# Performance work log

Measured on AMD Instinct MI355X. Metric: run time of the kernel, lower is better.

## Reference

```python
import jax, jax.numpy as jnp
import numpy as np

E = 80000   # number of directed edges
T = 80000   # number of triplets
HID = 256   # hidden_channels
INT = 64    # int_emb_size == num_bilinear
NR = 6      # num_radial
NS = 7      # num_spherical
BD = 8      # basis_emb_size_dist
BA = 8      # basis_emb_size_angle


def swish(x):
    return x * jax.nn.sigmoid(x)


def setup_inputs() -> dict:
    key = jax.random.key(0)
    ks = jax.random.split(key, 16)
    inp = {
        "x1": jax.random.normal(ks[0], (E, HID), dtype=jnp.float32),
        "rbf0": jax.random.normal(ks[1], (E, NR), dtype=jnp.float32),
        "sbf": jax.random.normal(ks[2], (T, NS * NR), dtype=jnp.float32),
        "t": jax.random.normal(ks[3], (T, NS * NS * NR), dtype=jnp.float32),
        "x_kj": jax.random.normal(ks[4], (E, HID), dtype=jnp.float32),
        "x_ji": jax.random.normal(ks[5], (E, HID), dtype=jnp.float32),
        "idx_kj": jax.random.randint(ks[6], (T,), 0, E, dtype=jnp.int32),
        "idx_ji": jax.random.randint(ks[7], (T,), 0, E, dtype=jnp.int32),
        # weights stored [in, out] so y = x @ W (torch Linear uses weight.T)
        "W_rbf1": jax.random.normal(ks[8], (NR, BD), dtype=jnp.float32) * 0.3,
        "W_rbf2": jax.random.normal(ks[9], (BD, HID), dtype=jnp.float32) * 0.3,
        "W_sbf1": jax.random.normal(ks[10], (NS * NR, BA), dtype=jnp.float32) * 0.15,
        "W_sbf2": jax.random.normal(ks[11], (BA, INT), dtype=jnp.float32) * 0.3,
        "W_t1": jax.random.normal(ks[12], (NS * NS * NR, INT), dtype=jnp.float32) * 0.06,
        "W_down": jax.random.normal(ks[13], (HID, INT), dtype=jnp.float32) * 0.06,
        "W_up": jax.random.normal(ks[14], (INT, HID), dtype=jnp.float32) * 0.12,
        # bilinear weight W: [int_emb, num_bilinear, int_emb], std = 2/int_emb
        "W_bil": jax.random.normal(ks[15], (INT, INT, INT), dtype=jnp.float32) * (2.0 / INT),
    }
    return inp


def reference(x1, rbf0, sbf, t, x_kj, x_ji, idx_kj, idx_ji,
              W_rbf1, W_rbf2, W_sbf1, W_sbf2, W_t1, W_down, W_up, W_bil):
    # rbf projection: [E, NR] -> [E, HID]
    rbf = (rbf0 @ W_rbf1) @ W_rbf2
    xk = x_kj * rbf                          # [E, HID]
    xk = swish(xk @ W_down)                  # [E, INT]
    # sbf projection: [T, NS*NR] -> [T, INT]
    s = (sbf @ W_sbf1) @ W_sbf2
    xk = xk[idx_kj] * s                      # gather to triplets: [T, INT]
    tt = t @ W_t1                            # [T, INT] (num_bilinear dim)
    # bilinear: 'wj,wl,ijl->wi' with W_bil [INT(i), INT(j), INT(l)]
    a = jnp.einsum('wj,ijl->wil', tt, W_bil)  # [T, INT, INT]
    out_t = jnp.einsum('wil,wl->wi', a, xk)   # [T, INT]
    # scatter-add triplets back to edges
    agg = jax.ops.segment_sum(out_t, idx_ji, num_segments=x1.shape[0])  # [E, INT]
    return swish(agg @ W_up)                  # [E, HID]
```

## Files before the change

### kernel.cpp

```cpp
#include <hip/hip_runtime.h>
#include <hip/hip_fp16.h>

#define E_N 80000
#define T_N 80000

typedef _Float16 h4 __attribute__((ext_vector_type(4)));
typedef _Float16 h8 __attribute__((ext_vector_type(8)));
typedef float    f4 __attribute__((ext_vector_type(4)));
typedef float    f2 __attribute__((ext_vector_type(2)));
typedef unsigned int u4 __attribute__((ext_vector_type(4)));

static __device__ __forceinline__ float swishf(float x) {
    return x / (1.0f + __expf(-x));
}

__global__ __launch_bounds__(256) void kp_pack(const float* __restrict__ Wb,
                                               h8* __restrict__ wpack) {
    int g = blockIdx.x * 256 + threadIdx.x;
    int i    = ((g >> 6) & 3) * 16 + (g & 15);
    int c    = (g >> 8) & 1;
    int j    = g >> 9;
    int quad = (g >> 4) & 3;
    int l0   = c * 32 + quad * 8;
    const float* src = Wb + ((i * 64 + j) << 6) + l0;
    h8 v;
#pragma unroll
    for (int u = 0; u < 8; ++u) v[u] = (_Float16)src[u];
    wpack[g] = v;
}

__global__ __launch_bounds__(256) void kpack_w(const float* __restrict__ src,
                                               h8* __restrict__ dst,
                                               int Ksrc, int N, int NT) {
    int g = blockIdx.x * 256 + threadIdx.x;
    int lane = g & 63, frag = g >> 6;
    int nt = frag % NT, kt = frag / NT;
    int quad = (lane >> 4);
    int n = nt * 16 + (lane & 15);
    int k0 = kt * 32 + quad * 8;
    h8 v;
#pragma unroll
    for (int u = 0; u < 8; ++u) {
        int k = k0 + u;
        v[u] = (k < Ksrc) ? (_Float16)src[(size_t)k * N + n] : (_Float16)0.0f;
    }
    dst[g] = v;
}

__global__ __launch_bounds__(256) void k1_down(const float* __restrict__ rbf0,
                                               const float* __restrict__ xkj,
                                               const float* __restrict__ W_rbf1,
                                               const float* __restrict__ W_rbf2,
                                               const h8* __restrict__ wpd,
                                               _Float16* __restrict__ xke) {
    int tid = threadIdx.x;
    int lane = tid & 63, wv = tid >> 6;
    int m = lane & 15, quad = lane >> 4;
    int rowb = blockIdx.x * 128 + wv * 32;

    float r8[2][8];
#pragma unroll
    for (int rt = 0; rt < 2; ++rt) {
        int r = rowb + rt * 16 + m;
        float rv[6];
#pragma unroll
        for (int q = 0; q < 6; ++q) rv[q] = rbf0[(size_t)r * 6 + q];
#pragma unroll
        for (int p = 0; p < 8; ++p) {
            float s = 0.f;
#pragma unroll
            for (int q = 0; q < 6; ++q) s += rv[q] * W_rbf1[q * 8 + p];
            r8[rt][p] = s;
        }
    }

    f4 acc[2][4] = {};
    for (int kb = 0; kb < 4; ++kb) {
#pragma unroll
        for (int kt = 0; kt < 2; ++kt) {
            int k0 = kb * 64 + kt * 32 + quad * 8;
            f4 w2lo[8], w2hi[8];
#pragma unroll
            for (int p = 0; p < 8; ++p) {
                w2lo[p] = *(const f4*)(W_rbf2 + p * 256 + k0);
                w2hi[p] = *(const f4*)(W_rbf2 + p * 256 + k0 + 4);
            }
            h8 afrag[2];
#pragma unroll
            for (int rt = 0; rt < 2; ++rt) {
                size_t base = (size_t)(rowb + rt * 16 + m) * 256 + k0;
                f4 xlo = *(const f4*)(xkj + base);
                f4 xhi = *(const f4*)(xkj + base + 4);
                f4 rlo = {}, rhi = {};
#pragma unroll
                for (int p = 0; p < 8; ++p) {
                    rlo += r8[rt][p] * w2lo[p];
                    rhi += r8[rt][p] * w2hi[p];
                }
                rlo *= xlo; rhi *= xhi;
                h8 a;
#pragma unroll
                for (int u = 0; u < 4; ++u) {
                    a[u]     = (_Float16)rlo[u];
                    a[u + 4] = (_Float16)rhi[u];
                }
                afrag[rt] = a;
            }
#pragma unroll
            for (int nt = 0; nt < 4; ++nt) {
                h8 b = wpd[(((kb * 2 + kt) * 4 + nt) << 6) + lane];
#pragma unroll
                for (int rt = 0; rt < 2; ++rt)
                    acc[rt][nt] = __builtin_amdgcn_mfma_f32_16x16x32_f16(afrag[rt], b, acc[rt][nt], 0, 0, 0);
            }
        }
    }

#pragma unroll
    for (int rt = 0; rt < 2; ++rt)
#pragma unroll
        for (int nt = 0; nt < 4; ++nt)
#pragma unroll
            for (int rr = 0; rr < 4; ++rr) {
                int row = rowb + rt * 16 + quad * 4 + rr;
                xke[(size_t)row * 64 + nt * 16 + m] = (_Float16)swishf(acc[rt][nt][rr]);
            }
}

__global__ __launch_bounds__(256) void kb1_tproj(const float* __restrict__ tin,
                                                 const h8* __restrict__ wpt,
                                                 _Float16* __restrict__ ttb) {
    int tid = threadIdx.x;
    int lane = tid & 63, wv = tid >> 6;
    int m = lane & 15, quad = lane >> 4;
    int rowb = blockIdx.x * 128 + wv * 32;

    f4 acc[2][4] = {};
    for (int ktg = 0; ktg < 10; ++ktg) {
        int k0 = ktg * 32 + quad * 8;
        h8 afrag[2];
#pragma unroll
        for (int rt = 0; rt < 2; ++rt) {
            size_t base = (size_t)(rowb + rt * 16 + m) * 294 + k0;
            h8 a;
            if (k0 + 8 <= 294) {
                f2 t0 = *(const f2*)(tin + base);
                f2 t1 = *(const f2*)(tin + base + 2);
                f2 t2 = *(const f2*)(tin + base + 4);
                f2 t3 = *(const f2*)(tin + base + 6);
                a[0] = (_Float16)t0[0]; a[1] = (_Float16)t0[1];
                a[2] = (_Float16)t1[0]; a[3] = (_Float16)t1[1];
                a[4] = (_Float16)t2[0]; a[5] = (_Float16)t2[1];
                a[6] = (_Float16)t3[0]; a[7] = (_Float16)t3[1];
            } else {
#pragma unroll
                for (int u = 0; u < 8; ++u) {
                    int k = k0 + u;
                    a[u] = (k < 294) ? (_Float16)tin[base + u] : (_Float16)0.0f;
                }
            }
            afrag[rt] = a;
        }
#pragma unroll
        for (int nt = 0; nt < 4; ++nt) {
            h8 b = wpt[((ktg * 4 + nt) << 6) + lane];
#pragma unroll
            for (int rt = 0; rt < 2; ++rt)
                acc[rt][nt] = __builtin_amdgcn_mfma_f32_16x16x32_f16(afrag[rt], b, acc[rt][nt], 0, 0, 0);
        }
    }

#pragma unroll
    for (int rt = 0; rt < 2; ++rt)
#pragma unroll
        for (int nt = 0; nt < 4; ++nt)
#pragma unroll
            for (int rr = 0; rr < 4; ++rr) {
                int row = rowb + rt * 16 + quad * 4 + rr;
                ttb[(size_t)row * 64 + nt * 16 + m] = (_Float16)acc[rt][nt][rr];
            }
}

__global__ __launch_bounds__(256) void kb2_gather(const float* __restrict__ sbf,
                                                  const float* __restrict__ W_sbf1,
                                                  const float* __restrict__ W_sbf2,
                                                  const _Float16* __restrict__ xke,
                                                  const int* __restrict__ idx_kj,
                                                  _Float16* __restrict__ xkt) {
    __shared__ float sbfL[32 * 42];
    __shared__ float midL[32 * 8];
    int tid = threadIdx.x;
    int row0 = blockIdx.x * 32;
    for (int i = tid; i < 32 * 42; i += 256)
        sbfL[i] = sbf[(size_t)row0 * 42 + i];
    __syncthreads();
    {
        int r = tid >> 3, p = tid & 7;
        float mm = 0.f;
#pragma unroll
        for (int q = 0; q < 42; ++q) mm += sbfL[r * 42 + q] * W_sbf1[q * 8 + p];
        midL[r * 8 + p] = mm;
    }
    __syncthreads();
    int r = tid >> 3;
    int c0 = (tid & 7) * 8;
    int w = row0 + r;
    int e = idx_kj[w];
    f4 sa = {}, sb = {};
#pragma unroll
    for (int p = 0; p < 8; ++p) {
        float mm = midL[r * 8 + p];
        sa += mm * *(const f4*)(W_sbf2 + (p << 6) + c0);
        sb += mm * *(const f4*)(W_sbf2 + (p << 6) + c0 + 4);
    }
    h8 xv = *(const h8*)(xke + (size_t)e * 64 + c0);
    h8 o;
#pragma unroll
    for (int u = 0; u < 4; ++u) {
        o[u]     = (_Float16)((float)xv[u]     * sa[u]);
        o[u + 4] = (_Float16)((float)xv[u + 4] * sb[u]);
    }
    *(h8*)(xkt + (size_t)w * 64 + c0) = o;
}

__global__ __launch_bounds__(256, 2) void kb3_bilinear(const _Float16* __restrict__ xkt,
                                                       const _Float16* __restrict__ ttp,
                                                       const h8* __restrict__ wpack,
                                                       const int* __restrict__ idx_ji,
                                                       float* __restrict__ agg) {
    __shared__ _Float16 xktL[256 * 72];
    __shared__ _Float16 ttL[256 * 72];
    int tid = threadIdx.x;
    int lane = tid & 63, wv = tid >> 6;
    int qrow = lane & 15, quad = lane >> 4;
    int row0 = blockIdx.x * 256;
    int jlo = blockIdx.y * 32;

#pragma unroll
    for (int pass = 0; pass < 8; ++pass) {
        int r = pass * 32 + (tid >> 3);
        int part = tid & 7;
        int gr = row0 + r;
        u4 vx = {0, 0, 0, 0}, vt = {0, 0, 0, 0};
        if (gr < T_N) {
            vx = *(const u4*)(xkt + (size_t)gr * 64 + part * 8);
            vt = *(const u4*)(ttp + (size_t)gr * 64 + part * 8);
        }
        *(u4*)&xktL[r * 72 + part * 8] = vx;
        *(u4*)&ttL[r * 72 + part * 8] = vt;
    }
    __syncthreads();

    int wrow = wv * 64;
    h8 xa[4][2];
#pragma unroll
    for (int rt = 0; rt < 4; ++rt)
#pragma unroll
        for (int c = 0; c < 2; ++c)
            xa[rt][c] = *(const h8*)&xktL[(wrow + rt * 16 + qrow) * 72 + c * 32 + quad * 8];

    f4 acc[4][4] = {};
    for (int j = jlo; j < jlo + 32; ++j) {
        h8 bf[2][4];
#pragma unroll
        for (int c = 0; c < 2; ++c)
#pragma unroll
            for (int nt = 0; nt < 4; ++nt)
                bf[c][nt] = wpack[(((j * 2 + c) * 4 + nt) << 6) + lane];
        _Float16 tv[4];
#pragma unroll
        for (int rt = 0; rt < 4; ++rt)
            tv[rt] = ttL[(wrow + rt * 16 + qrow) * 72 + j];
#pragma unroll
        for (int rt = 0; rt < 4; ++rt) {
            h8 t8 = {tv[rt], tv[rt], tv[rt], tv[rt], tv[rt], tv[rt], tv[rt], tv[rt]};
            h8 a0 = xa[rt][0] * t8;
            h8 a1 = xa[rt][1] * t8;
#pragma unroll
            for (int nt = 0; nt < 4; ++nt) {
                acc[rt][nt] = __builtin_amdgcn_mfma_f32_16x16x32_f16(a0, bf[0][nt], acc[rt][nt], 0, 0, 0);
                acc[rt][nt] = __builtin_amdgcn_mfma_f32_16x16x32_f16(a1, bf[1][nt], acc[rt][nt], 0, 0, 0);
            }
        }
    }

#pragma unroll
    for (int rt = 0; rt < 4; ++rt) {
#pragma unroll
        for (int rr = 0; rr < 4; ++rr) {
            int w = row0 + wrow + rt * 16 + quad * 4 + rr;
            if (w < T_N) {
                int e = idx_ji[w];
                float* dst = agg + (size_t)e * 64 + qrow;
#pragma unroll
                for (int nt = 0; nt < 4; ++nt)
                    atomicAdd(dst + nt * 16, acc[rt][nt][rr]);
            }
        }
    }
}

__global__ __launch_bounds__(256) void k4_up(const float* __restrict__ agg,
                                             const h8* __restrict__ wpu,
                                             float* __restrict__ out) {
    int tid = threadIdx.x;
    int lane = tid & 63, wv = tid >> 6;
    int m = lane & 15, quad = lane >> 4;
    int rowb = blockIdx.x * 64 + wv * 16;

    f4 acc[16] = {};
#pragma unroll
    for (int kt = 0; kt < 2; ++kt) {
        const float* ap = agg + (size_t)(rowb + m) * 64 + kt * 32 + quad * 8;
        f4 alo = *(const f4*)ap;
        f4 ahi = *(const f4*)(ap + 4);
        h8 a;
#pragma unroll
        for (int u = 0; u < 4; ++u) {
            a[u]     = (_Float16)alo[u];
            a[u + 4] = (_Float16)ahi[u];
        }
#pragma unroll
        for (int nt = 0; nt < 16; ++nt) {
            h8 b = wpu[((kt * 16 + nt) << 6) + lane];
            acc[nt] = __builtin_amdgcn_mfma_f32_16x16x32_f16(a, b, acc[nt], 0, 0, 0);
        }
    }

#pragma unroll
    for (int nt = 0; nt < 16; ++nt)
#pragma unroll
        for (int rr = 0; rr < 4; ++rr) {
            int row = rowb + quad * 4 + rr;
            out[(size_t)row * 256 + nt * 16 + m] = swishf(acc[nt][rr]);
        }
}

extern "C" void kernel_launch(void* const* d_in, const int* in_sizes, int n_in,
                              void* d_out, int out_size, void* d_ws, size_t ws_size,
                              hipStream_t stream) {
    const float* rbf0   = (const float*)d_in[1];
    const float* sbf    = (const float*)d_in[2];
    const float* tin    = (const float*)d_in[3];
    const float* xkj    = (const float*)d_in[4];
    const int*   idx_kj = (const int*)d_in[6];
    const int*   idx_ji = (const int*)d_in[7];
    const float* W_rbf1 = (const float*)d_in[8];
    const float* W_rbf2 = (const float*)d_in[9];
    const float* W_sbf1 = (const float*)d_in[10];
    const float* W_sbf2 = (const float*)d_in[11];
    const float* W_t1   = (const float*)d_in[12];
    const float* W_down = (const float*)d_in[13];
    const float* W_up   = (const float*)d_in[14];
    const float* W_bil  = (const float*)d_in[15];

    char* ws = (char*)d_ws;
    _Float16* xke = (_Float16*)ws;
    float*    agg = (float*)(ws + 10240000);
    h8* wpack_bil = (h8*)(ws + 30720000);
    h8* wpd       = (h8*)(ws + 31244288);
    h8* wpt       = (h8*)(ws + 31277056);
    h8* wpu       = (h8*)(ws + 31318016);
    _Float16* ttb = (_Float16*)d_out;
    _Float16* xkt = (_Float16*)((char*)d_out + 10240000);
    float*    out = (float*)d_out;

    kp_pack<<<128, 256, 0, stream>>>(W_bil, wpack_bil);
    kpack_w<<<8,  256, 0, stream>>>(W_down, wpd, 256, 64, 4);
    kpack_w<<<10, 256, 0, stream>>>(W_t1,   wpt, 294, 64, 4);
    kpack_w<<<8,  256, 0, stream>>>(W_up,   wpu, 64, 256, 16);
    k1_down<<<625, 256, 0, stream>>>(rbf0, xkj, W_rbf1, W_rbf2, wpd, xke);
    kb1_tproj<<<625, 256, 0, stream>>>(tin, wpt, ttb);
    kb2_gather<<<2500, 256, 0, stream>>>(sbf, W_sbf1, W_sbf2, xke, idx_kj, xkt);
    hipMemsetAsync(agg, 0, (size_t)E_N * 64 * 4, stream);
    kb3_bilinear<<<dim3(313, 2), 256, 0, stream>>>(xkt, ttb, wpack_bil, idx_ji, agg);
    k4_up<<<1250, 256, 0, stream>>>(agg, wpu, out);
}
```

Baseline: 479.8 us.

## Merge weight-pack kernels, drop LDS staging in bilinear, flatten down-proj loop

Packs all four weight tensors in one kernel launch instead of four, which cuts launch overhead. The bilinear kernel now uses 128-thread blocks that read xkt and tt fragments straight from global memory instead of staging them in shared memory, and it loads eight tt values at a time per row. The bounds check on T goes away because 625*128 rows covers T exactly. k1_down unrolls its K loop fully under a launch bound of 4, and the memset moves earlier in the stream. The risks are higher register pressure and uncoalesced global reads in the bilinear kernel.

```diff
diff --git a/kernel.cpp b/kernel.cpp
--- a/kernel.cpp
+++ b/kernel.cpp
@@ -14,25 +14,9 @@
     return x / (1.0f + __expf(-x));
 }
 
-__global__ __launch_bounds__(256) void kp_pack(const float* __restrict__ Wb,
-                                               h8* __restrict__ wpack) {
-    int g = blockIdx.x * 256 + threadIdx.x;
-    int i    = ((g >> 6) & 3) * 16 + (g & 15);
-    int c    = (g >> 8) & 1;
-    int j    = g >> 9;
-    int quad = (g >> 4) & 3;
-    int l0   = c * 32 + quad * 8;
-    const float* src = Wb + ((i * 64 + j) << 6) + l0;
-    h8 v;
-#pragma unroll
-    for (int u = 0; u < 8; ++u) v[u] = (_Float16)src[u];
-    wpack[g] = v;
-}
-
-__global__ __launch_bounds__(256) void kpack_w(const float* __restrict__ src,
-                                               h8* __restrict__ dst,
-                                               int Ksrc, int N, int NT) {
-    int g = blockIdx.x * 256 + threadIdx.x;
+static __device__ __forceinline__ void pack_w_dev(const float* __restrict__ src,
+                                                  h8* __restrict__ dst,
+                                                  int g, int Ksrc, int N, int NT) {
     int lane = g & 63, frag = g >> 6;
     int nt = frag % NT, kt = frag / NT;
     int quad = (lane >> 4);
@@ -47,12 +31,38 @@
     dst[g] = v;
 }
 
-__global__ __launch_bounds__(256) void k1_down(const float* __restrict__ rbf0,
-                                               const float* __restrict__ xkj,
-                                               const float* __restrict__ W_rbf1,
-                                               const float* __restrict__ W_rbf2,
-                                               const h8* __restrict__ wpd,
-                                               _Float16* __restrict__ xke) {
+__global__ __launch_bounds__(256) void kpack_all(const float* __restrict__ Wb,  h8* __restrict__ wbil,
+                                                 const float* __restrict__ Wd,  h8* __restrict__ wpd,
+                                                 const float* __restrict__ Wt,  h8* __restrict__ wpt,
+                                                 const float* __restrict__ Wu,  h8* __restrict__ wpu) {
+    int b = blockIdx.x, tid = threadIdx.x;
+    if (b < 128) {
+        int g = b * 256 + tid;
+        int i    = ((g >> 6) & 3) * 16 + (g & 15);
+        int c    = (g >> 8) & 1;
+        int j    = g >> 9;
+        int quad = (g >> 4) & 3;
+        int l0   = c * 32 + quad * 8;
+        const float* src = Wb + ((i * 64 + j) << 6) + l0;
+        h8 v;
+#pragma unroll
+        for (int u = 0; u < 8; ++u) v[u] = (_Float16)src[u];
+        wbil[g] = v;
+    } else if (b < 136) {
+        pack_w_dev(Wd, wpd, (b - 128) * 256 + tid, 256, 64, 4);
+    } else if (b < 146) {
+        pack_w_dev(Wt, wpt, (b - 136) * 256 + tid, 294, 64, 4);
+    } else {
+        pack_w_dev(Wu, wpu, (b - 146) * 256 + tid, 64, 256, 16);
+    }
+}
+
+__global__ __launch_bounds__(256, 4) void k1_down(const float* __restrict__ rbf0,
+                                                  const float* __restrict__ xkj,
+                                                  const float* __restrict__ W_rbf1,
+                                                  const float* __restrict__ W_rbf2,
+                                                  const h8* __restrict__ wpd,
+                                                  _Float16* __restrict__ xke) {
     int tid = threadIdx.x;
     int lane = tid & 63, wv = tid >> 6;
     int m = lane & 15, quad = lane >> 4;
@@ -75,44 +85,35 @@
     }
 
     f4 acc[2][4] = {};
-    for (int kb = 0; kb < 4; ++kb) {
-#pragma unroll
-        for (int kt = 0; kt < 2; ++kt) {
-            int k0 = kb * 64 + kt * 32 + quad * 8;
-            f4 w2lo[8], w2hi[8];
+#pragma unroll
+    for (int kb = 0; kb < 8; ++kb) {
+        int k0 = kb * 32 + quad * 8;
+        h8 afrag[2];
+#pragma unroll
+        for (int rt = 0; rt < 2; ++rt) {
+            f4 rlo = {}, rhi = {};
 #pragma unroll
             for (int p = 0; p < 8; ++p) {
-                w2lo[p] = *(const f4*)(W_rbf2 + p * 256 + k0);
-                w2hi[p] = *(const f4*)(W_rbf2 + p * 256 + k0 + 4);
-            }
-            h8 afrag[2];
-#pragma unroll
-            for (int rt = 0; rt < 2; ++rt) {
-                size_t base = (size_t)(rowb + rt * 16 + m) * 256 + k0;
-                f4 xlo = *(const f4*)(xkj + base);
-                f4 xhi = *(const f4*)(xkj + base + 4);
-                f4 rlo = {}, rhi = {};
-#pragma unroll
-                for (int p = 0; p < 8; ++p) {
-                    rlo += r8[rt][p] * w2lo[p];
-                    rhi += r8[rt][p] * w2hi[p];
-                }
-                rlo *= xlo; rhi *= xhi;
-                h8 a;
-#pragma unroll
-                for (int u = 0; u < 4; ++u) {
-                    a[u]     = (_Float16)rlo[u];
-                    a[u + 4] = (_Float16)rhi[u];
-                }
-                afrag[rt] = a;
-            }
-#pragma unroll
-            for (int nt = 0; nt < 4; ++nt) {
-                h8 b = wpd[(((kb * 2 + kt) * 4 + nt) << 6) + lane];
-#pragma unroll
-                for (int rt = 0; rt < 2; ++rt)
-                    acc[rt][nt] = __builtin_amdgcn_mfma_f32_16x16x32_f16(afrag[rt], b, acc[rt][nt], 0, 0, 0);
-            }
+                rlo += r8[rt][p] * *(const f4*)(W_rbf2 + p * 256 + k0);
+                rhi += r8[rt][p] * *(const f4*)(W_rbf2 + p * 256 + k0 + 4);
+            }
+            size_t base = (size_t)(rowb + rt * 16 + m) * 256 + k0;
+            f4 xlo = *(const f4*)(xkj + base);
+            f4 xhi = *(const f4*)(xkj + base + 4);
+            rlo *= xlo; rhi *= xhi;
+            h8 a;
+#pragma unroll
+            for (int u = 0; u < 4; ++u) {
+                a[u]     = (_Float16)rlo[u];
+                a[u + 4] = (_Float16)rhi[u];
+            }
+            afrag[rt] = a;
+        }
+#pragma unroll
+        for (int nt = 0; nt < 4; ++nt) {
+            h8 b = wpd[((kb * 4 + nt) << 6) + lane];
+            acc[0][nt] = __builtin_amdgcn_mfma_f32_16x16x32_f16(afrag[0], b, acc[0][nt], 0, 0, 0);
+            acc[1][nt] = __builtin_amdgcn_mfma_f32_16x16x32_f16(afrag[1], b, acc[1][nt], 0, 0, 0);
         }
     }
 
@@ -223,79 +224,67 @@
     *(h8*)(xkt + (size_t)w * 64 + c0) = o;
 }
 
-__global__ __launch_bounds__(256, 2) void kb3_bilinear(const _Float16* __restrict__ xkt,
+__global__ __launch_bounds__(128, 3) void kb3_bilinear(const _Float16* __restrict__ xkt,
                                                        const _Float16* __restrict__ ttp,
                                                        const h8* __restrict__ wpack,
                                                        const int* __restrict__ idx_ji,
                                                        float* __restrict__ agg) {
-    __shared__ _Float16 xktL[256 * 72];
-    __shared__ _Float16 ttL[256 * 72];
     int tid = threadIdx.x;
     int lane = tid & 63, wv = tid >> 6;
     int qrow = lane & 15, quad = lane >> 4;
-    int row0 = blockIdx.x * 256;
+    int row0 = blockIdx.x * 128 + wv * 64;
     int jlo = blockIdx.y * 32;
 
-#pragma unroll
-    for (int pass = 0; pass < 8; ++pass) {
-        int r = pass * 32 + (tid >> 3);
-        int part = tid & 7;
-        int gr = row0 + r;
-        u4 vx = {0, 0, 0, 0}, vt = {0, 0, 0, 0};
-        if (gr < T_N) {
-            vx = *(const u4*)(xkt + (size_t)gr * 64 + part * 8);
-            vt = *(const u4*)(ttp + (size_t)gr * 64 + part * 8);
-        }
-        *(u4*)&xktL[r * 72 + part * 8] = vx;
-        *(u4*)&ttL[r * 72 + part * 8] = vt;
-    }
-    __syncthreads();
-
-    int wrow = wv * 64;
     h8 xa[4][2];
 #pragma unroll
-    for (int rt = 0; rt < 4; ++rt)
-#pragma unroll
-        for (int c = 0; c < 2; ++c)
-            xa[rt][c] = *(const h8*)&xktL[(wrow + rt * 16 + qrow) * 72 + c * 32 + quad * 8];
+    for (int rt = 0; rt < 4; ++rt) {
+        const _Float16* rp = xkt + (size_t)(row0 + rt * 16 + qrow) * 64 + quad * 8;
+        xa[rt][0] = *(const h8*)rp;
+        xa[rt][1] = *(const h8*)(rp + 32);
+    }
 
     f4 acc[4][4] = {};
-    for (int j = jlo; j < jlo + 32; ++j) {
-        h8 bf[2][4];
-#pragma unroll
-        for (int c = 0; c < 2; ++c)
+#pragma unroll
+    for (int jg = 0; jg < 4; ++jg) {
+        h8 tg[4];
+#pragma unroll
+        for (int rt = 0; rt < 4; ++rt)
+            tg[rt] = *(const h8*)(ttp + (size_t)(row0 + rt * 16 + qrow) * 64 + jlo + jg * 8);
+#pragma unroll
+        for (int ju = 0; ju < 8; ++ju) {
+            int j = jlo + jg * 8 + ju;
+            const h8* wj = wpack + (((size_t)j * 8) << 6) + lane;
+            h8 b0[4], b1[4];
+#pragma unroll
+            for (int nt = 0; nt < 4; ++nt) {
+                b0[nt] = wj[nt << 6];
+                b1[nt] = wj[(4 + nt) << 6];
+            }
+#pragma unroll
+            for (int rt = 0; rt < 4; ++rt) {
+                _Float16 tv = tg[rt][ju];
+                h8 t8 = {tv, tv, tv, tv, tv, tv, tv, tv};
+                h8 a0 = xa[rt][0] * t8;
+                h8 a1 = xa[rt][1] * t8;
+#pragma unroll
+                for (int nt = 0; nt < 4; ++nt) {
+                    acc[rt][nt] = __builtin_amdgcn_mfma_f32_16x16x32_f16(a0, b0[nt], acc[rt][nt], 0, 0, 0);
+                    acc[rt][nt] = __builtin_amdgcn_mfma_f32_16x16x32_f16(a1, b1[nt], acc[rt][nt], 0, 0, 0);
+                }
+            }
+        }
+    }
+
+#pragma unroll
+    for (int rt = 0; rt < 4; ++rt) {
+#pragma unroll
+        for (int rr = 0; rr < 4; ++rr) {
+            int w = row0 + rt * 16 + quad * 4 + rr;
+            int e = idx_ji[w];
+            float* dst = agg + (size_t)e * 64 + qrow;
 #pragma unroll
             for (int nt = 0; nt < 4; ++nt)
-                bf[c][nt] = wpack[(((j * 2 + c) * 4 + nt) << 6) + lane];
-        _Float16 tv[4];
-#pragma unroll
-        for (int rt = 0; rt < 4; ++rt)
-            tv[rt] = ttL[(wrow + rt * 16 + qrow) * 72 + j];
-#pragma unroll
-        for (int rt = 0; rt < 4; ++rt) {
-            h8 t8 = {tv[rt], tv[rt], tv[rt], tv[rt], tv[rt], tv[rt], tv[rt], tv[rt]};
-            h8 a0 = xa[rt][0] * t8;
-            h8 a1 = xa[rt][1] * t8;
-#pragma unroll
-            for (int nt = 0; nt < 4; ++nt) {
-                acc[rt][nt] = __builtin_amdgcn_mfma_f32_16x16x32_f16(a0, bf[0][nt], acc[rt][nt], 0, 0, 0);
-                acc[rt][nt] = __builtin_amdgcn_mfma_f32_16x16x32_f16(a1, bf[1][nt], acc[rt][nt], 0, 0, 0);
-            }
-        }
-    }
-
-#pragma unroll
-    for (int rt = 0; rt < 4; ++rt) {
-#pragma unroll
-        for (int rr = 0; rr < 4; ++rr) {
-            int w = row0 + wrow + rt * 16 + quad * 4 + rr;
-            if (w < T_N) {
-                int e = idx_ji[w];
-                float* dst = agg + (size_t)e * 64 + qrow;
-#pragma unroll
-                for (int nt = 0; nt < 4; ++nt)
-                    atomicAdd(dst + nt * 16, acc[rt][nt][rr]);
-            }
+                atomicAdd(dst + nt * 16, acc[rt][nt][rr]);
         }
     }
 }
@@ -365,14 +354,11 @@
     _Float16* xkt = (_Float16*)((char*)d_out + 10240000);
     float*    out = (float*)d_out;
 
-    kp_pack<<<128, 256, 0, stream>>>(W_bil, wpack_bil);
-    kpack_w<<<8,  256, 0, stream>>>(W_down, wpd, 256, 64, 4);
-    kpack_w<<<10, 256, 0, stream>>>(W_t1,   wpt, 294, 64, 4);
-    kpack_w<<<8,  256, 0, stream>>>(W_up,   wpu, 64, 256, 16);
+    hipMemsetAsync(agg, 0, (size_t)E_N * 64 * 4, stream);
+    kpack_all<<<154, 256, 0, stream>>>(W_bil, wpack_bil, W_down, wpd, W_t1, wpt, W_up, wpu);
     k1_down<<<625, 256, 0, stream>>>(rbf0, xkj, W_rbf1, W_rbf2, wpd, xke);
     kb1_tproj<<<625, 256, 0, stream>>>(tin, wpt, ttb);
     kb2_gather<<<2500, 256, 0, stream>>>(sbf, W_sbf1, W_sbf2, xke, idx_kj, xkt);
-    hipMemsetAsync(agg, 0, (size_t)E_N * 64 * 4, stream);
-    kb3_bilinear<<<dim3(313, 2), 256, 0, stream>>>(xkt, ttb, wpack_bil, idx_ji, agg);
+    kb3_bilinear<<<dim3(625, 2), 128, 0, stream>>>(xkt, ttb, wpack_bil, idx_ji, agg);
     k4_up<<<1250, 256, 0, stream>>>(agg, wpu, out);
 }
```

New measurement: 475.8 us. About the same (-0.8%).
